# Performance work log

Hardware: AMD Instinct MI355X
Metric: run time of the kernel (lower is better)

The kernel has to match this reference:

```python
import jax, jax.numpy as jnp
import numpy as np

SIG = 10.0
C = 0.0
STD = 1.0
N_ATOMS = 21
DESC = N_ATOMS * (N_ATOMS - 1) // 2  # 210
N_TRAIN = 4096
M = 128


def setup_inputs() -> dict:
    key = jax.random.key(0)
    k1, k2, k3 = jax.random.split(key, 3)
    # Cartesian coordinates, spread out so interatomic distances are O(1)
    Rs = jax.random.normal(k1, (M, N_ATOMS, 3), dtype=jnp.float32) * 2.0
    # training descriptors are inverse distances -> positive
    xs_train = jax.random.uniform(k2, (N_TRAIN, DESC), dtype=jnp.float32)
    Jx_alphas = jax.random.normal(k3, (N_TRAIN, DESC), dtype=jnp.float32)
    return {"Rs": Rs, "xs_train": xs_train, "Jx_alphas": Jx_alphas}


def reference(Rs, xs_train, Jx_alphas):
    sig, c, std = SIG, C, STD
    n_atoms = Rs.shape[1]
    i, j = np.tril_indices(n_atoms, k=-1)  # static index pattern

    # pairwise displacement vectors, [M, N, N, 3]
    diffs = Rs[:, :, None, :] - Rs[:, None, :, :]
    # gather strict lower triangle first, then take norm (avoids norm-at-zero on diag)
    d_vec = diffs[:, i, j, :]                      # [M, desc, 3]
    r = jnp.linalg.norm(d_vec, axis=-1)            # [M, desc]
    xs = 1.0 / r                                   # inverse-distance descriptor

    q = np.sqrt(5.0) / sig
    # [M, T, desc] broadcast diff vs training descriptors
    x_diffs = (q * xs)[:, None, :] - q * xs_train[None, :, :]
    x_dists = jnp.linalg.norm(x_diffs, axis=-1)    # [M, T]
    exp_xs = (5.0 / (3.0 * sig ** 2)) * jnp.exp(-x_dists)
    dot_x_diff_Jx = jnp.einsum('mtd,td->mt', x_diffs, Jx_alphas)
    exp_xs_1_x_dists = exp_xs * (1.0 + x_dists)

    # force pieces in descriptor space
    F1s_x = jnp.einsum('mt,mtd->md', exp_xs * dot_x_diff_Jx, x_diffs)
    F2s_x = exp_xs_1_x_dists @ Jx_alphas           # [M, desc]
    Fs_x = (F1s_x - F2s_x) * std

    # expand_tril(Fs_x) / dists**3, with zero diagonal (torch sets diag dists=inf)
    coef = Fs_x / r ** 3                           # [M, desc]
    full = jnp.zeros((Rs.shape[0], n_atoms, n_atoms), dtype=Rs.dtype)
    full = full.at[:, i, j].set(coef).at[:, j, i].set(coef)
    # sum over first atom axis (torch dim=1)
    Fs = jnp.einsum('mab,mabc->mbc', full, diffs)  # [M, N, 3]

    Es = jnp.sum(exp_xs_1_x_dists * dot_x_diff_Jx, axis=-1) / q
    Es = c + Es * std
    return Es, Fs
```

## Files before the change

### kernel.cpp

```cpp
#include <hip/hip_runtime.h>
#include <math.h>

#define NATOMS 21
#define DESC 210
#define DPAD 224
#define P4 112
#define NTRAIN 4096
#define NM 128

#define CC 0.0f
#define STDC 1.0f
#define QS 0.22360679774997896f
#define KE 0.016666666666666666f

__device__ __forceinline__ void gll16(const void* gptr, void* lptr) {
    __builtin_amdgcn_global_load_lds(
        (__attribute__((address_space(1))) void*)gptr,
        (__attribute__((address_space(3))) void*)lptr,
        16, 0, 0);
}

__device__ __forceinline__ void pair_ij(int p, int& i, int& j) {
    int ii = (int)((1.0f + sqrtf(1.0f + 8.0f * (float)p)) * 0.5f);
    while (ii * (ii - 1) / 2 > p) --ii;
    while ((ii + 1) * ii / 2 <= p) ++ii;
    i = ii;
    j = p - ii * (ii - 1) / 2;
}

__global__ __launch_bounds__(256, 2) void k_prep(const float* __restrict__ Rs,
                                                 const float* __restrict__ xs_train,
                                                 const float* __restrict__ Jx,
                                                 float2* __restrict__ xj2,
                                                 float* __restrict__ aT,
                                                 float* __restrict__ aPf,
                                                 float* __restrict__ asq,
                                                 float* __restrict__ bsqPart,
                                                 float* __restrict__ cjPart,
                                                 float* __restrict__ Fzero) {
    __shared__ float smem[2 * 32 * 65 + 8];
    const int tid = threadIdx.x;
    const int bid = blockIdx.x;
    {
        const int z = bid * 256 + tid;
        if (z < 2 * 26880) Fzero[z] = 0.0f;
    }
    if (bid < 448) {
        float* ldsX = smem;
        float* ldsJ = smem + 32 * 65;
        const int bx = bid & 63;
        const int by = bid >> 6;
        const int t0 = bx * 64;
        const int d0 = by * 32;
        #pragma unroll
        for (int k = 0; k < 8; ++k) {
            const int idx = tid + k * 256;
            const int tt = idx >> 5;
            const int dd = idx & 31;
            const int d = d0 + dd;
            float xv = 0.0f, jv = 0.0f;
            if (d < DESC) {
                xv = QS * xs_train[(t0 + tt) * DESC + d];
                jv = Jx[(t0 + tt) * DESC + d];
            }
            ldsX[dd * 65 + tt] = xv;
            ldsJ[dd * 65 + tt] = jv;
        }
        __syncthreads();
        #pragma unroll
        for (int k = 0; k < 8; ++k) {
            const int idx = tid + k * 256;
            const int tt = idx >> 5;
            const int dd = idx & 31;
            xj2[(t0 + tt) * 256 + d0 + dd] =
                make_float2(ldsX[dd * 65 + tt], ldsJ[dd * 65 + tt]);
        }
        if (tid < 64) {
            float sb = 0.0f, sc = 0.0f;
            #pragma unroll
            for (int dd = 0; dd < 32; ++dd) {
                const float b = ldsX[dd * 65 + tid];
                const float jj = ldsJ[dd * 65 + tid];
                sb = fmaf(b, b, sb);
                sc = fmaf(b, jj, sc);
            }
            bsqPart[by * NTRAIN + t0 + tid] = sb;
            cjPart[by * NTRAIN + t0 + tid] = sc;
        }
    } else {
        const int m = bid - 448;
        float* R = smem;
        float* red = smem + 64;
        if (tid < NATOMS * 3) R[tid] = Rs[m * NATOMS * 3 + tid];
        __syncthreads();
        float a2 = 0.0f;
        if (tid < DPAD) {
            float a = 0.0f;
            if (tid < DESC) {
                int i, j;
                pair_ij(tid, i, j);
                const float dx = R[i * 3 + 0] - R[j * 3 + 0];
                const float dy = R[i * 3 + 1] - R[j * 3 + 1];
                const float dz = R[i * 3 + 2] - R[j * 3 + 2];
                a = QS / sqrtf(dx * dx + dy * dy + dz * dz);
            }
            aT[tid * NM + m] = a;
            aPf[(tid >> 1) * 256 + m * 2 + (tid & 1)] = a;
            a2 = a * a;
        }
        #pragma unroll
        for (int off = 32; off > 0; off >>= 1) a2 += __shfl_down(a2, off, 64);
        if ((tid & 63) == 0) red[tid >> 6] = a2;
        __syncthreads();
        if (tid == 0) asq[m] = red[0] + red[1] + red[2] + red[3];
    }
}

__global__ __launch_bounds__(256, 4) void k_pass1(const float2* __restrict__ xj2,
                                                  const float2* __restrict__ aP,
                                                  const float* __restrict__ asq,
                                                  const float* __restrict__ bsqPart,
                                                  const float* __restrict__ cjPart,
                                                  float2* __restrict__ w12T,
                                                  float* __restrict__ EsPart,
                                                  float* __restrict__ S1Part) {
    const int tid = threadIdx.x;
    const int bid = blockIdx.x;
    const int ml = tid & 127;
    const int tgu = __builtin_amdgcn_readfirstlane(tid >> 7);
    const int t0 = bid * 4 + tgu * 2;

    float P[2] = {0.f, 0.f};
    float Q[2] = {0.f, 0.f};
    const float2* ap = aP + ml;
    const float4* r0 = (const float4*)(xj2 + (size_t)(t0 + 0) * 256);
    const float4* r1 = (const float4*)(xj2 + (size_t)(t0 + 1) * 256);

    #pragma unroll 8
    for (int p = 0; p < P4; ++p) {
        const float2 a = ap[p * 128];
        const float4 b0 = r0[p];
        const float4 b1 = r1[p];
        P[0] = fmaf(a.x, b0.x, P[0]); P[0] = fmaf(a.y, b0.z, P[0]);
        Q[0] = fmaf(a.x, b0.y, Q[0]); Q[0] = fmaf(a.y, b0.w, Q[0]);
        P[1] = fmaf(a.x, b1.x, P[1]); P[1] = fmaf(a.y, b1.z, P[1]);
        Q[1] = fmaf(a.x, b1.y, Q[1]); Q[1] = fmaf(a.y, b1.w, Q[1]);
    }

    const float asqv = asq[ml];
    float es = 0.f, s1 = 0.f;
    #pragma unroll
    for (int j = 0; j < 2; ++j) {
        const int t = t0 + j;
        float bsqv = 0.f, cjv = 0.f;
        #pragma unroll
        for (int by = 0; by < 7; ++by) {
            bsqv += bsqPart[by * NTRAIN + t];
            cjv += cjPart[by * NTRAIN + t];
        }
        float dist2 = asqv + bsqv - 2.0f * P[j];
        dist2 = fmaxf(dist2, 0.0f);
        const float x = sqrtf(dist2);
        const float e = KE * expf(-x);
        const float dotv = Q[j] - cjv;
        const float w1v = e * dotv;
        const float w2v = e * (1.0f + x);
        w12T[t * NM + ml] = make_float2(w1v, w2v);
        es += w2v * dotv;
        s1 += w1v;
    }
    __shared__ float esL[2][128], s1L[2][128];
    esL[tgu][ml] = es;
    s1L[tgu][ml] = s1;
    __syncthreads();
    if (tid < 128) {
        EsPart[bid * NM + tid] = esL[0][tid] + esL[1][tid];
        S1Part[bid * NM + tid] = s1L[0][tid] + s1L[1][tid];
    }
}

__global__ __launch_bounds__(256, 2) void k_pass2(const float2* __restrict__ xj2,
                                                  const float2* __restrict__ w12T,
                                                  float* __restrict__ F1acc,
                                                  float* __restrict__ F2acc) {
    const int tid = threadIdx.x;
    const int bid = blockIdx.x;
    const int bx = (bid & 7) + 8 * (bid >> 7);
    const int my = (bid >> 3) & 15;
    const int t0 = bx * 128;
    const int m0 = my * 8;

    __shared__ __align__(16) float2 wS2[128][8];
    __shared__ __align__(16) float2 xjS[3][8][256];

    {
        #pragma unroll
        for (int k = 0; k < 2; ++k) {
            const int idx = tid + k * 256;
            gll16(&w12T[(t0 + (idx >> 2)) * NM + m0 + 2 * (idx & 3)],
                  &reinterpret_cast<float4*>(wS2)[idx]);
        }
        const int row = tid >> 7;
        const int col = tid & 127;
        #pragma unroll
        for (int k = 0; k < 4; ++k)
            gll16(&xj2[(t0 + row + 2 * k) * 256 + 2 * col],
                  &xjS[0][row + 2 * k][2 * col]);
        #pragma unroll
        for (int k = 0; k < 4; ++k)
            gll16(&xj2[(t0 + 8 + row + 2 * k) * 256 + 2 * col],
                  &xjS[1][row + 2 * k][2 * col]);
    }

    const int d = (tid < DESC) ? tid : 0;
    float G1[8] = {0.f, 0.f, 0.f, 0.f, 0.f, 0.f, 0.f, 0.f};
    float G2[8] = {0.f, 0.f, 0.f, 0.f, 0.f, 0.f, 0.f, 0.f};

    for (int c = 0; c < 16; ++c) {
        if (c < 15) {
            asm volatile("s_waitcnt vmcnt(4) lgkmcnt(0)" ::: "memory");
        } else {
            asm volatile("s_waitcnt vmcnt(0) lgkmcnt(0)" ::: "memory");
        }
        __builtin_amdgcn_s_barrier();
        __builtin_amdgcn_sched_barrier(0);
        const float2* xjC = &xjS[c % 3][0][0];
        #pragma unroll
        for (int tt = 0; tt < 8; ++tt) {
            const int tb = c * 8 + tt;
            const float2 xj = xjC[tt * 256 + d];
            const float4 wa = *reinterpret_cast<const float4*>(&wS2[tb][0]);
            const float4 wb = *reinterpret_cast<const float4*>(&wS2[tb][2]);
            const float4 wc = *reinterpret_cast<const float4*>(&wS2[tb][4]);
            const float4 wd = *reinterpret_cast<const float4*>(&wS2[tb][6]);
            G1[0] = fmaf(wa.x, xj.x, G1[0]); G2[0] = fmaf(wa.y, xj.y, G2[0]);
            G1[1] = fmaf(wa.z, xj.x, G1[1]); G2[1] = fmaf(wa.w, xj.y, G2[1]);
            G1[2] = fmaf(wb.x, xj.x, G1[2]); G2[2] = fmaf(wb.y, xj.y, G2[2]);
            G1[3] = fmaf(wb.z, xj.x, G1[3]); G2[3] = fmaf(wb.w, xj.y, G2[3]);
            G1[4] = fmaf(wc.x, xj.x, G1[4]); G2[4] = fmaf(wc.y, xj.y, G2[4]);
            G1[5] = fmaf(wc.z, xj.x, G1[5]); G2[5] = fmaf(wc.w, xj.y, G2[5]);
            G1[6] = fmaf(wd.x, xj.x, G1[6]); G2[6] = fmaf(wd.y, xj.y, G2[6]);
            G1[7] = fmaf(wd.z, xj.x, G1[7]); G2[7] = fmaf(wd.w, xj.y, G2[7]);
        }
        if (c < 14) {
            const int row = tid >> 7;
            const int col = tid & 127;
            float2* dst = &xjS[(c + 2) % 3][0][0];
            #pragma unroll
            for (int k = 0; k < 4; ++k)
                gll16(&xj2[(t0 + (c + 2) * 8 + row + 2 * k) * 256 + 2 * col],
                      &dst[(row + 2 * k) * 256 + 2 * col]);
        }
    }

    if (tid < DESC) {
        #pragma unroll
        for (int mi = 0; mi < 8; ++mi) {
            atomicAdd(&F1acc[(m0 + mi) * DESC + tid], G1[mi]);
            atomicAdd(&F2acc[(m0 + mi) * DESC + tid], G2[mi]);
        }
    }
}

__global__ __launch_bounds__(256) void k_final(const float* __restrict__ Rs,
                                               const float* __restrict__ aT,
                                               const float* __restrict__ EsPart,
                                               const float* __restrict__ S1Part,
                                               const float* __restrict__ F1acc,
                                               const float* __restrict__ F2acc,
                                               float* __restrict__ out) {
    const int m = blockIdx.x;
    __shared__ float R[NATOMS * 3];
    __shared__ float FsL[NATOMS * 3];
    __shared__ float redE[4], redS[4];
    __shared__ float sEs, sS1;
    const int tid = threadIdx.x;
    float esp = 0.f, s1p = 0.f;
    #pragma unroll
    for (int k = 0; k < 4; ++k) {
        esp += EsPart[(tid + k * 256) * NM + m];
        s1p += S1Part[(tid + k * 256) * NM + m];
    }
    #pragma unroll
    for (int off = 32; off > 0; off >>= 1) {
        esp += __shfl_down(esp, off, 64);
        s1p += __shfl_down(s1p, off, 64);
    }
    if ((tid & 63) == 0) { redE[tid >> 6] = esp; redS[tid >> 6] = s1p; }
    if (tid < NATOMS * 3) {
        R[tid] = Rs[m * NATOMS * 3 + tid];
        FsL[tid] = 0.0f;
    }
    __syncthreads();
    if (tid == 0) {
        sEs = redE[0] + redE[1] + redE[2] + redE[3];
        sS1 = redS[0] + redS[1] + redS[2] + redS[3];
    }
    __syncthreads();
    if (tid < DESC) {
        int i, j;
        pair_ij(tid, i, j);
        const float dx = R[i * 3 + 0] - R[j * 3 + 0];
        const float dy = R[i * 3 + 1] - R[j * 3 + 1];
        const float dz = R[i * 3 + 2] - R[j * 3 + 2];
        const float r2 = dx * dx + dy * dy + dz * dz;
        const float rinv = 1.0f / sqrtf(r2);
        const float a = aT[tid * NM + m];
        const float F1 = a * sS1 - F1acc[m * DESC + tid];
        const float Fx = (F1 - F2acc[m * DESC + tid]) * STDC;
        const float coef = Fx * (rinv * rinv * rinv);
        atomicAdd(&FsL[j * 3 + 0], coef * dx);
        atomicAdd(&FsL[j * 3 + 1], coef * dy);
        atomicAdd(&FsL[j * 3 + 2], coef * dz);
        atomicAdd(&FsL[i * 3 + 0], -coef * dx);
        atomicAdd(&FsL[i * 3 + 1], -coef * dy);
        atomicAdd(&FsL[i * 3 + 2], -coef * dz);
    }
    __syncthreads();
    if (tid < NATOMS * 3) out[NM + m * NATOMS * 3 + tid] = FsL[tid];
    if (tid == 0) out[m] = CC + (sEs / QS) * STDC;
}

extern "C" void kernel_launch(void* const* d_in, const int* in_sizes, int n_in,
                              void* d_out, int out_size, void* d_ws, size_t ws_size,
                              hipStream_t stream) {
    const float* Rs = (const float*)d_in[0];
    const float* xs_train = (const float*)d_in[1];
    const float* Jx = (const float*)d_in[2];
    float* out = (float*)d_out;
    float* ws = (float*)d_ws;

    float* F1acc = ws;
    float* F2acc = ws + 26880;
    float* bsqPart = ws + 53760;
    float* cjPart = ws + 82432;
    float* aT = ws + 111104;
    float* asq = ws + 139776;
    float* aPf = ws + 139904;
    float* EsPart = ws + 168576;
    float* S1Part = ws + 299648;
    float2* w12T = (float2*)(ws + 430720);
    float2* xj2 = (float2*)(ws + 1479296);

    k_prep<<<576, 256, 0, stream>>>(Rs, xs_train, Jx, xj2, aT, aPf, asq,
                                    bsqPart, cjPart, F1acc);
    k_pass1<<<1024, 256, 0, stream>>>(xj2, (const float2*)aPf, asq, bsqPart, cjPart,
                                      w12T, EsPart, S1Part);
    k_pass2<<<512, 256, 0, stream>>>(xj2, w12T, F1acc, F2acc);
    k_final<<<NM, 256, 0, stream>>>(Rs, aT, EsPart, S1Part, F1acc, F2acc, out);
}
```

Before: 61.90 us.

## Widen pass2 tile to 16 samples per block and double-buffer xj chunks

The F1/F2 accumulation kernel now gives each block 16 molecules instead of 8, halving the grid to 256 blocks and halving how often each xj chunk is reloaded from global memory. The triple-buffered prefetch with partial vmcnt waits becomes a simple double buffer that issues the next chunk after a full wait and barrier. This trades fewer redundant loads and atomics for less parallelism (256 blocks on a 256-CU part), more registers per thread, and less latency hiding, since each chunk has only one compute step to arrive.

```diff
diff --git a/kernel.cpp b/kernel.cpp
--- a/kernel.cpp
+++ b/kernel.cpp
@@ -185,77 +185,70 @@
                                                   float* __restrict__ F2acc) {
     const int tid = threadIdx.x;
     const int bid = blockIdx.x;
-    const int bx = (bid & 7) + 8 * (bid >> 7);
-    const int my = (bid >> 3) & 15;
+    const int bx = (bid & 7) + 8 * (bid >> 6);
+    const int mg = (bid >> 3) & 7;
     const int t0 = bx * 128;
-    const int m0 = my * 8;
-
-    __shared__ __align__(16) float2 wS2[128][8];
-    __shared__ __align__(16) float2 xjS[3][8][256];
-
-    {
-        #pragma unroll
-        for (int k = 0; k < 2; ++k) {
-            const int idx = tid + k * 256;
-            gll16(&w12T[(t0 + (idx >> 2)) * NM + m0 + 2 * (idx & 3)],
-                  &reinterpret_cast<float4*>(wS2)[idx]);
-        }
-        const int row = tid >> 7;
-        const int col = tid & 127;
-        #pragma unroll
-        for (int k = 0; k < 4; ++k)
-            gll16(&xj2[(t0 + row + 2 * k) * 256 + 2 * col],
-                  &xjS[0][row + 2 * k][2 * col]);
-        #pragma unroll
-        for (int k = 0; k < 4; ++k)
-            gll16(&xj2[(t0 + 8 + row + 2 * k) * 256 + 2 * col],
-                  &xjS[1][row + 2 * k][2 * col]);
+    const int m0 = mg * 16;
+
+    __shared__ __align__(16) float2 wS2[128][16];
+    __shared__ __align__(16) float2 xjS[2][8][256];
+
+    #pragma unroll
+    for (int k = 0; k < 4; ++k) {
+        const int idx = tid + k * 256;
+        const int tt = idx >> 3;
+        const int f = idx & 7;
+        gll16((const float4*)(w12T + (size_t)(t0 + tt) * NM + m0) + f,
+              reinterpret_cast<float4*>(wS2) + idx);
+    }
+    #pragma unroll
+    for (int k = 0; k < 4; ++k) {
+        const int idx = tid + k * 256;
+        const int row = idx >> 7;
+        const int col = idx & 127;
+        gll16(&xj2[(size_t)(t0 + row) * 256 + 2 * col], &xjS[0][row][2 * col]);
     }
 
     const int d = (tid < DESC) ? tid : 0;
-    float G1[8] = {0.f, 0.f, 0.f, 0.f, 0.f, 0.f, 0.f, 0.f};
-    float G2[8] = {0.f, 0.f, 0.f, 0.f, 0.f, 0.f, 0.f, 0.f};
+    float G1[16], G2[16];
+    #pragma unroll
+    for (int i = 0; i < 16; ++i) { G1[i] = 0.f; G2[i] = 0.f; }
 
     for (int c = 0; c < 16; ++c) {
-        if (c < 15) {
-            asm volatile("s_waitcnt vmcnt(4) lgkmcnt(0)" ::: "memory");
-        } else {
-            asm volatile("s_waitcnt vmcnt(0) lgkmcnt(0)" ::: "memory");
-        }
+        asm volatile("s_waitcnt vmcnt(0) lgkmcnt(0)" ::: "memory");
         __builtin_amdgcn_s_barrier();
         __builtin_amdgcn_sched_barrier(0);
-        const float2* xjC = &xjS[c % 3][0][0];
+        if (c < 15) {
+            float2* dst = &xjS[(c + 1) & 1][0][0];
+            #pragma unroll
+            for (int k = 0; k < 4; ++k) {
+                const int idx = tid + k * 256;
+                const int row = idx >> 7;
+                const int col = idx & 127;
+                gll16(&xj2[(size_t)(t0 + (c + 1) * 8 + row) * 256 + 2 * col],
+                      &dst[row * 256 + 2 * col]);
+            }
+        }
+        const float2* xjC = &xjS[c & 1][0][0];
         #pragma unroll
         for (int tt = 0; tt < 8; ++tt) {
             const int tb = c * 8 + tt;
             const float2 xj = xjC[tt * 256 + d];
-            const float4 wa = *reinterpret_cast<const float4*>(&wS2[tb][0]);
-            const float4 wb = *reinterpret_cast<const float4*>(&wS2[tb][2]);
-            const float4 wc = *reinterpret_cast<const float4*>(&wS2[tb][4]);
-            const float4 wd = *reinterpret_cast<const float4*>(&wS2[tb][6]);
-            G1[0] = fmaf(wa.x, xj.x, G1[0]); G2[0] = fmaf(wa.y, xj.y, G2[0]);
-            G1[1] = fmaf(wa.z, xj.x, G1[1]); G2[1] = fmaf(wa.w, xj.y, G2[1]);
-            G1[2] = fmaf(wb.x, xj.x, G1[2]); G2[2] = fmaf(wb.y, xj.y, G2[2]);
-            G1[3] = fmaf(wb.z, xj.x, G1[3]); G2[3] = fmaf(wb.w, xj.y, G2[3]);
-            G1[4] = fmaf(wc.x, xj.x, G1[4]); G2[4] = fmaf(wc.y, xj.y, G2[4]);
-            G1[5] = fmaf(wc.z, xj.x, G1[5]); G2[5] = fmaf(wc.w, xj.y, G2[5]);
-            G1[6] = fmaf(wd.x, xj.x, G1[6]); G2[6] = fmaf(wd.y, xj.y, G2[6]);
-            G1[7] = fmaf(wd.z, xj.x, G1[7]); G2[7] = fmaf(wd.w, xj.y, G2[7]);
-        }
-        if (c < 14) {
-            const int row = tid >> 7;
-            const int col = tid & 127;
-            float2* dst = &xjS[(c + 2) % 3][0][0];
+            const float4* wrow = reinterpret_cast<const float4*>(&wS2[tb][0]);
             #pragma unroll
-            for (int k = 0; k < 4; ++k)
-                gll16(&xj2[(t0 + (c + 2) * 8 + row + 2 * k) * 256 + 2 * col],
-                      &dst[(row + 2 * k) * 256 + 2 * col]);
+            for (int k = 0; k < 8; ++k) {
+                const float4 w = wrow[k];
+                G1[2 * k]     = fmaf(w.x, xj.x, G1[2 * k]);
+                G2[2 * k]     = fmaf(w.y, xj.y, G2[2 * k]);
+                G1[2 * k + 1] = fmaf(w.z, xj.x, G1[2 * k + 1]);
+                G2[2 * k + 1] = fmaf(w.w, xj.y, G2[2 * k + 1]);
+            }
         }
     }
 
     if (tid < DESC) {
         #pragma unroll
-        for (int mi = 0; mi < 8; ++mi) {
+        for (int mi = 0; mi < 16; ++mi) {
             atomicAdd(&F1acc[(m0 + mi) * DESC + tid], G1[mi]);
             atomicAdd(&F2acc[(m0 + mi) * DESC + tid], G2[mi]);
         }
@@ -346,6 +339,6 @@
                                     bsqPart, cjPart, F1acc);
     k_pass1<<<1024, 256, 0, stream>>>(xj2, (const float2*)aPf, asq, bsqPart, cjPart,
                                       w12T, EsPart, S1Part);
-    k_pass2<<<512, 256, 0, stream>>>(xj2, w12T, F1acc, F2acc);
+    k_pass2<<<256, 256, 0, stream>>>(xj2, w12T, F1acc, F2acc);
     k_final<<<NM, 256, 0, stream>>>(Rs, aT, EsPart, S1Part, F1acc, F2acc, out);
 }
```

Measured after the change: 71.96 us. +16.3%, slower.
